# Optimization experiments

Measured on AMD Instinct MI355X. Metric: run time of the kernel, lower is better.

## Reference

```python
import jax, jax.numpy as jnp
from jax import lax
import numpy as np

B, DIM, H, W = 8, 192, 128, 128
HEADS = 4


def setup_inputs() -> dict:
    key = jax.random.key(0)
    k1, k2, k3, k4 = jax.random.split(key, 4)
    x = jax.random.normal(k1, (B, DIM, H, W), dtype=jnp.float32)
    w_qkv = jax.random.normal(k2, (2 * DIM, DIM), dtype=jnp.float32) * 0.05
    w_dw = jax.random.normal(k3, (2 * DIM, 1, 3, 3), dtype=jnp.float32) * 0.1
    w_proj = jax.random.normal(k4, (DIM, DIM), dtype=jnp.float32) * 0.05
    temperature = jnp.ones((HEADS, 1, 1), dtype=jnp.float32)
    return {"x": x, "w_qkv": w_qkv, "w_dw": w_dw, "w_proj": w_proj, "temperature": temperature}


def reference(x, w_qkv, w_dw, w_proj, temperature):
    b, c, h, w = x.shape
    heads = temperature.shape[0]
    head_c = c // heads
    # 1x1 conv: dim -> 2*dim
    qkv = jnp.einsum('oc,bchw->bohw', w_qkv, x)
    # 3x3 depthwise conv over 2*dim channels
    qkv = lax.conv_general_dilated(
        qkv, w_dw, window_strides=(1, 1), padding='SAME',
        feature_group_count=2 * c,
        dimension_numbers=('NCHW', 'OIHW', 'NCHW'))
    q, v = jnp.split(qkv, 2, axis=1)
    # [b, heads, head_c, h*w]
    q = q.reshape(b, heads, head_c, h * w)
    v = v.reshape(b, heads, head_c, h * w)
    # L2-normalize q over spatial dim; k = q
    q = q / jnp.linalg.norm(q, axis=-1, keepdims=True)
    # channel-wise attention: [b, heads, head_c, head_c]
    attn = jnp.einsum('bhcn,bhdn->bhcd', q, q) * temperature[None]
    attn = jax.nn.softmax(attn, axis=-1)
    out = jnp.einsum('bhcd,bhdn->bhcn', attn, v)
    out = out.reshape(b, c, h, w)
    # 1x1 projection
    return jnp.einsum('oc,bchw->bohw', w_proj, out)
```

## Files before the change

kernel.cpp:

```cpp
#include <hip/hip_runtime.h>

#define BB 8
#define CC 192
#define C2 384
#define HH 128
#define WW 128
#define NN 16384
#define NHEADS 4
#define HC 48
#define LTK 196
#define LTK2 98

typedef float f32x4 __attribute__((ext_vector_type(4)));
typedef float f32x16 __attribute__((ext_vector_type(16)));
typedef short s16x4 __attribute__((ext_vector_type(4)));
typedef short s16x8 __attribute__((ext_vector_type(8)));
typedef unsigned short u16;
typedef u16 u16x4 __attribute__((ext_vector_type(4)));
typedef u16 u16x8 __attribute__((ext_vector_type(8)));
typedef unsigned int u32;

__device__ __forceinline__ float bfu2f(u32 u16v) {
  return __uint_as_float(u16v << 16);
}
__device__ __forceinline__ u16 f2bfu(float f) {
  u32 u = __float_as_uint(f);
  return (u16)((u + 0x7fffu + ((u >> 16) & 1u)) >> 16);
}
__device__ __forceinline__ s16x8 ldpair(const u16* p) {
  s16x4 lo = *reinterpret_cast<const s16x4*>(p);
  s16x4 hi = *reinterpret_cast<const s16x4*>(p + 16);
  return __builtin_shufflevector(lo, hi, 0, 1, 2, 3, 4, 5, 6, 7);
}
__device__ __forceinline__ s16x8 ldb64pair(const u32* p) {
  s16x4 lo = *reinterpret_cast<const s16x4*>(p);
  s16x4 hi = *reinterpret_cast<const s16x4*>(p + 2);
  return __builtin_shufflevector(lo, hi, 0, 1, 2, 3, 4, 5, 6, 7);
}

__global__ __launch_bounds__(256) void k0_wcvt(const float* __restrict__ w,
                                               u16* __restrict__ wbf) {
  const int i = (blockIdx.x * 256 + threadIdx.x) * 4;
  f32x4 v = *reinterpret_cast<const f32x4*>(&w[i]);
  u16x4 o;
  o[0] = f2bfu(v[0]); o[1] = f2bfu(v[1]); o[2] = f2bfu(v[2]); o[3] = f2bfu(v[3]);
  *reinterpret_cast<u16x4*>(&wbf[i]) = o;
}

__global__ __launch_bounds__(512, 4) void k1_qkv(
    const float* __restrict__ x, const u16* __restrict__ wbf,
    u16* __restrict__ qkv) {
  const int bx = blockIdx.x;
  const int n0 = (((bx & 7) << 4) + (bx >> 3)) << 7;
  const int b  = blockIdx.y;
  __shared__ u16 Xs[128 * LTK];
  u32* Xsw = reinterpret_cast<u32*>(Xs);
  const int t = threadIdx.x, lane = t & 63;
  const int wid = t >> 6, wo = wid >> 1, wn = wid & 1;
  const int l31 = lane & 31, g2 = lane >> 5;

  {
    const int nq = t & 31, cr = t >> 5;
    const int kpb = cr >> 1;
    const int jh = cr & 1;
    const int prA = 2 * nq + jh;
    const int prB = 64 + 2 * nq + jh;
    const float* xb = x + (size_t)b * CC * NN + n0 + 4 * nq;
    #pragma unroll 6
    for (int i = 0; i < 12; ++i) {
      f32x4 v = *reinterpret_cast<const f32x4*>(xb + (size_t)(cr + 16 * i) * NN);
      u32 A  = (u32)f2bfu(v[0]) | ((u32)f2bfu(v[1]) << 16);
      u32 Bp = (u32)f2bfu(v[2]) | ((u32)f2bfu(v[3]) << 16);
      u32 oA = __shfl_xor(A, 32);
      u32 oB = __shfl_xor(Bp, 32);
      u32 va, vb;
      if (jh) {
        va = (oB & 0xffffu) | (Bp << 16);
        vb = (oB >> 16) | (Bp & 0xffff0000u);
      } else {
        va = (A & 0xffffu) | (oA << 16);
        vb = (A >> 16) | (oA & 0xffff0000u);
      }
      const int col = kpb + 8 * i;
      Xsw[prA * LTK2 + col] = va;
      Xsw[prB * LTK2 + col] = vb;
    }
  }
  __syncthreads();

  const int nb2 = wn * 32;
  const u32* browE = &Xsw[(nb2 + l31) * LTK2 + 4 * g2];
  const u32* browO = &Xsw[(64 + nb2 + l31) * LTK2 + 4 * g2];

  for (int ot = 0; ot < 3; ++ot) {
    const int o0 = ot * 128;
    const u16* wr = wbf + (size_t)(o0 + wo * 32 + l31) * CC + 8 * g2;

    s16x8 afA[6], afB[6];
    #pragma unroll
    for (int s = 0; s < 6; ++s) {
      afA[s] = *reinterpret_cast<const s16x8*>(wr + s * 32);
      afB[s] = *reinterpret_cast<const s16x8*>(wr + s * 32 + 16);
    }

    f32x16 accE, accO;
    #pragma unroll
    for (int e = 0; e < 16; ++e) { accE[e] = 0.f; accO[e] = 0.f; }

    #pragma unroll
    for (int s = 0; s < 6; ++s) {
      s16x8 bfE0 = ldb64pair(browE + 16 * s);
      s16x8 bfE1 = ldb64pair(browE + 16 * s + 8);
      s16x8 bfO0 = ldb64pair(browO + 16 * s);
      s16x8 bfO1 = ldb64pair(browO + 16 * s + 8);
      accE = __builtin_amdgcn_mfma_f32_32x32x16_bf16(afA[s], bfE0, accE, 0, 0, 0);
      accO = __builtin_amdgcn_mfma_f32_32x32x16_bf16(afA[s], bfO0, accO, 0, 0, 0);
      accE = __builtin_amdgcn_mfma_f32_32x32x16_bf16(afB[s], bfE1, accE, 0, 0, 0);
      accO = __builtin_amdgcn_mfma_f32_32x32x16_bf16(afB[s], bfO1, accO, 0, 0, 0);
    }
    #pragma unroll
    for (int r = 0; r < 16; ++r) {
      const int row = (r & 3) + 8 * (r >> 2) + 4 * g2;
      const u32 pk = (u32)f2bfu(accE[r]) | ((u32)f2bfu(accO[r]) << 16);
      *reinterpret_cast<u32*>(
          &qkv[((size_t)b * C2 + o0 + wo * 32 + row) * NN + n0 + wn * 64 + 2 * l31]) = pk;
    }
  }
}

__global__ __launch_bounds__(256) void k2_dw(
    const u16* __restrict__ qkv, const float* __restrict__ wdw,
    u16* __restrict__ out) {
  const int gid = blockIdx.x;
  const int rb = gid & 7;
  const int plane = gid >> 3;
  const int ch = plane % C2;
  const int t = threadIdx.x;
  const int row = rb * 16 + (t >> 4);
  const int x0 = (t & 15) * 8;
  const u16* p = qkv + (size_t)plane * NN;
  const float* wv = wdw + ch * 9;
  float o[8];
  #pragma unroll
  for (int j = 0; j < 8; ++j) o[j] = 0.f;
  #pragma unroll
  for (int dy = 0; dy < 3; ++dy) {
    const int yy = row + dy - 1;
    if ((unsigned)yy < (unsigned)HH) {
      const u16* rp = p + yy * WW;
      u16x8 m = *reinterpret_cast<const u16x8*>(&rp[x0]);
      float px[10];
      px[0] = (x0 > 0) ? bfu2f(rp[x0 - 1]) : 0.f;
      px[9] = (x0 < 120) ? bfu2f(rp[x0 + 8]) : 0.f;
      #pragma unroll
      for (int j = 0; j < 8; ++j) px[j + 1] = bfu2f(m[j]);
      const float w0 = wv[dy * 3 + 0], w1 = wv[dy * 3 + 1], w2 = wv[dy * 3 + 2];
      #pragma unroll
      for (int j = 0; j < 8; ++j)
        o[j] += w0 * px[j] + w1 * px[j + 1] + w2 * px[j + 2];
    }
  }
  u16x8 ov;
  #pragma unroll
  for (int j = 0; j < 8; ++j) ov[j] = f2bfu(o[j]);
  *reinterpret_cast<u16x8*>(&out[(size_t)plane * NN + row * WW + x0]) = ov;
}

__global__ __launch_bounds__(256) void k3_gram(
    const u16* __restrict__ qkvd, float* __restrict__ gpart) {
  const int bh = blockIdx.x, b = bh >> 2, h = bh & 3;
  const int chunk = blockIdx.y;
  const int t = threadIdx.x, lane = t & 63, wv = t >> 6;
  const int l15 = lane & 15, g = lane >> 4;
  __shared__ float red[4][2304];
  const u16* qb = qkvd + ((size_t)b * C2 + h * HC) * NN;

  f32x4 acc[3][3];
  #pragma unroll
  for (int i = 0; i < 3; ++i)
    #pragma unroll
    for (int j = 0; j < 3; ++j)
      #pragma unroll
      for (int e = 0; e < 4; ++e) acc[i][j][e] = 0.f;

  const int nbase = chunk * 1024 + wv * 256;
  #pragma unroll 2
  for (int st = 0; st < 8; ++st) {
    const int n = nbase + st * 32;
    s16x8 cf[3];
    #pragma unroll
    for (int i = 0; i < 3; ++i)
      cf[i] = ldpair(qb + (size_t)(i * 16 + l15) * NN + n + 4 * g);
    #pragma unroll
    for (int i = 0; i < 3; ++i)
      #pragma unroll
      for (int j = 0; j < 3; ++j)
        acc[i][j] = __builtin_amdgcn_mfma_f32_16x16x32_bf16(cf[i], cf[j], acc[i][j], 0, 0, 0);
  }
  #pragma unroll
  for (int i = 0; i < 3; ++i)
    #pragma unroll
    for (int j = 0; j < 3; ++j)
      #pragma unroll
      for (int r = 0; r < 4; ++r)
        red[wv][(i * 16 + 4 * g + r) * 48 + j * 16 + l15] = acc[i][j][r];
  __syncthreads();
  float* gp = gpart + ((size_t)bh * 16 + chunk) * 2304;
  for (int idx = t; idx < 2304; idx += 256)
    gp[idx] = red[0][idx] + red[1][idx] + red[2][idx] + red[3][idx];
}

__global__ __launch_bounds__(256) void k4_soft(
    const float* __restrict__ gpart, const float* __restrict__ temp,
    float* __restrict__ attn) {
  const int bh = blockIdx.x;
  const int h = bh & 3;
  const int t = threadIdx.x;
  __shared__ float G[2304];
  __shared__ float rn[48];
  for (int idx = t; idx < 2304; idx += 256) {
    float s = 0.f;
    #pragma unroll
    for (int c = 0; c < 16; ++c) s += gpart[((size_t)bh * 16 + c) * 2304 + idx];
    G[idx] = s;
  }
  __syncthreads();
  if (t < 48) rn[t] = rsqrtf(G[t * 48 + t]);
  __syncthreads();
  if (t < 48) {
    const float tm = temp[h];
    float v[48];
    float mx = -1e30f;
    #pragma unroll
    for (int j = 0; j < 48; ++j) {
      v[j] = G[t * 48 + j] * rn[t] * rn[j] * tm;
      mx = fmaxf(mx, v[j]);
    }
    float s = 0.f;
    #pragma unroll
    for (int j = 0; j < 48; ++j) { v[j] = expf(v[j] - mx); s += v[j]; }
    const float inv = 1.f / s;
    #pragma unroll
    for (int j = 0; j < 48; ++j)
      attn[(size_t)bh * 2304 + t * 48 + j] = v[j] * inv;
  }
}

__global__ __launch_bounds__(192) void k5_M(
    const float* __restrict__ wproj, const float* __restrict__ attn,
    u16* __restrict__ Mbf) {
  const int o = blockIdx.x;
  const int b = blockIdx.y;
  const int d = threadIdx.x;
  const int h = d / HC, dl = d % HC;
  const float* wrow = wproj + o * CC + h * HC;
  const float* at = attn + ((size_t)(b * NHEADS + h)) * 2304;
  float s = 0.f;
  #pragma unroll
  for (int c = 0; c < HC; ++c) s = fmaf(wrow[c], at[c * HC + dl], s);
  Mbf[((size_t)b * CC + o) * CC + d] = f2bfu(s);
}

__global__ __launch_bounds__(256, 4) void k6_out(
    const u16* __restrict__ Mbf, const u16* __restrict__ qkvd,
    float* __restrict__ out) {
  const int bx = blockIdx.x;
  const int n0 = (((bx & 7) << 4) + (bx >> 3)) << 7;
  const int b  = blockIdx.y;
  __shared__ u16 Vs[128 * LTK];
  u32* Vsw = reinterpret_cast<u32*>(Vs);
  const int t = threadIdx.x, lane = t & 63;
  const int wid = t >> 6, wo = wid >> 1, wn = wid & 1;
  const int l31 = lane & 31, g2 = lane >> 5;

  {
    const int nq = t & 31, cr = t >> 5;
    const int kpb = cr >> 1;
    const int jh = cr & 1;
    const int prA = 2 * nq + jh;
    const int prB = 64 + 2 * nq + jh;
    const u16* vbp = qkvd + ((size_t)b * C2 + CC) * NN + n0 + 4 * nq;
    #pragma unroll 6
    for (int i = 0; i < 24; ++i) {
      u16x4 m = *reinterpret_cast<const u16x4*>(vbp + (size_t)(cr + 8 * i) * NN);
      u32 A  = (u32)m[0] | ((u32)m[1] << 16);
      u32 Bp = (u32)m[2] | ((u32)m[3] << 16);
      u32 oA = __shfl_xor(A, 32);
      u32 oB = __shfl_xor(Bp, 32);
      u32 va, vb;
      if (jh) {
        va = (oB & 0xffffu) | (Bp << 16);
        vb = (oB >> 16) | (Bp & 0xffff0000u);
      } else {
        va = (A & 0xffffu) | (oA << 16);
        vb = (A >> 16) | (oA & 0xffff0000u);
      }
      const int col = kpb + 4 * i;
      Vsw[prA * LTK2 + col] = va;
      Vsw[prB * LTK2 + col] = vb;
    }
  }
  __syncthreads();

  const int nb2 = wn * 32;
  const u32* browE = &Vsw[(nb2 + l31) * LTK2 + 4 * g2];
  const u32* browO = &Vsw[(64 + nb2 + l31) * LTK2 + 4 * g2];
  const u16* Ab = Mbf + (size_t)b * CC * CC;

  for (int ot = 0; ot < 3; ++ot) {
    const int o0 = ot * 64;
    const u16* ar = Ab + (size_t)(o0 + wo * 32 + l31) * CC + 8 * g2;

    s16x8 afA[6], afB[6];
    #pragma unroll
    for (int s = 0; s < 6; ++s) {
      afA[s] = *reinterpret_cast<const s16x8*>(ar + s * 32);
      afB[s] = *reinterpret_cast<const s16x8*>(ar + s * 32 + 16);
    }

    f32x16 accE, accO;
    #pragma unroll
    for (int e = 0; e < 16; ++e) { accE[e] = 0.f; accO[e] = 0.f; }

    #pragma unroll
    for (int s = 0; s < 6; ++s) {
      s16x8 bfE0 = ldb64pair(browE + 16 * s);
      s16x8 bfE1 = ldb64pair(browE + 16 * s + 8);
      s16x8 bfO0 = ldb64pair(browO + 16 * s);
      s16x8 bfO1 = ldb64pair(browO + 16 * s + 8);
      accE = __builtin_amdgcn_mfma_f32_32x32x16_bf16(afA[s], bfE0, accE, 0, 0, 0);
      accO = __builtin_amdgcn_mfma_f32_32x32x16_bf16(afA[s], bfO0, accO, 0, 0, 0);
      accE = __builtin_amdgcn_mfma_f32_32x32x16_bf16(afB[s], bfE1, accE, 0, 0, 0);
      accO = __builtin_amdgcn_mfma_f32_32x32x16_bf16(afB[s], bfO1, accO, 0, 0, 0);
    }
    #pragma unroll
    for (int r = 0; r < 16; ++r) {
      const int row = (r & 3) + 8 * (r >> 2) + 4 * g2;
      float2 st;
      st.x = accE[r];
      st.y = accO[r];
      *reinterpret_cast<float2*>(
          &out[((size_t)b * CC + o0 + wo * 32 + row) * NN + n0 + wn * 64 + 2 * l31]) = st;
    }
  }
}

extern "C" void kernel_launch(void* const* d_in, const int* in_sizes, int n_in,
                              void* d_out, int out_size, void* d_ws, size_t ws_size,
                              hipStream_t stream) {
  const float* x      = (const float*)d_in[0];
  const float* w_qkv  = (const float*)d_in[1];
  const float* w_dw   = (const float*)d_in[2];
  const float* w_proj = (const float*)d_in[3];
  const float* temp   = (const float*)d_in[4];
  float* out = (float*)d_out;

  const size_t OFF_QKV   = 0;
  const size_t OFF_QKVD  = 100663296ULL;
  const size_t OFF_GPART = 201326592ULL;
  const size_t OFF_ATTN  = 206045184ULL;
  const size_t OFF_M     = 206340096ULL;
  const size_t OFF_WBF   = 206929920ULL;
  const size_t NEEDED    = 207077376ULL;
  if (ws_size < NEEDED) return;

  char* ws = (char*)d_ws;
  u16* qkv   = (u16*)(ws + OFF_QKV);
  u16* qkvd  = (u16*)(ws + OFF_QKVD);
  float* gpart = (float*)(ws + OFF_GPART);
  float* attn  = (float*)(ws + OFF_ATTN);
  u16* Mbf   = (u16*)(ws + OFF_M);
  u16* wbf   = (u16*)(ws + OFF_WBF);

  k0_wcvt<<<dim3(72), 256, 0, stream>>>(w_qkv, wbf);
  k1_qkv <<<dim3(128, 8), 512, 0, stream>>>(x, wbf, qkv);
  k2_dw  <<<dim3(BB * C2 * 8), 256, 0, stream>>>(qkv, w_dw, qkvd);
  k3_gram<<<dim3(BB * NHEADS, 16), 256, 0, stream>>>(qkvd, gpart);
  k4_soft<<<dim3(BB * NHEADS), 256, 0, stream>>>(gpart, temp, attn);
  k5_M   <<<dim3(CC, BB), 192, 0, stream>>>(w_proj, attn, Mbf);
  k6_out <<<dim3(128, 8), 256, 0, stream>>>(Mbf, qkvd, out);
}
```

Before: 214.8 us.

## Double k1 spatial tile to 256 columns with 1024-thread blocks and simpler staging

The QKV 1x1-conv kernel now processes 256 spatial positions per block with 16 waves instead of 128 positions with 8 waves, halving the grid. This spreads each weight-fragment load over twice as many columns. The X staging loop is rewritten to load two channel rows per thread and pack channel pairs directly, which removes the cross-lane shuffles. In exchange, LDS use per block doubles to about 100KB, which limits occupancy to one block per CU, and the grid of 512 blocks may fill the GPU less evenly.

```diff
diff --git a/kernel.cpp b/kernel.cpp
--- a/kernel.cpp
+++ b/kernel.cpp
@@ -47,50 +47,41 @@
   *reinterpret_cast<u16x4*>(&wbf[i]) = o;
 }
 
-__global__ __launch_bounds__(512, 4) void k1_qkv(
+__global__ __launch_bounds__(1024, 4) void k1_qkv(
     const float* __restrict__ x, const u16* __restrict__ wbf,
     u16* __restrict__ qkv) {
   const int bx = blockIdx.x;
-  const int n0 = (((bx & 7) << 4) + (bx >> 3)) << 7;
+  const int n0 = (((bx & 7) << 3) + (bx >> 3)) << 8;
   const int b  = blockIdx.y;
-  __shared__ u16 Xs[128 * LTK];
+  __shared__ u16 Xs[256 * LTK];
   u32* Xsw = reinterpret_cast<u32*>(Xs);
   const int t = threadIdx.x, lane = t & 63;
-  const int wid = t >> 6, wo = wid >> 1, wn = wid & 1;
+  const int wid = t >> 6, wo = wid >> 2, wn = wid & 3;
   const int l31 = lane & 31, g2 = lane >> 5;
 
   {
-    const int nq = t & 31, cr = t >> 5;
-    const int kpb = cr >> 1;
-    const int jh = cr & 1;
-    const int prA = 2 * nq + jh;
-    const int prB = 64 + 2 * nq + jh;
-    const float* xb = x + (size_t)b * CC * NN + n0 + 4 * nq;
-    #pragma unroll 6
-    for (int i = 0; i < 12; ++i) {
-      f32x4 v = *reinterpret_cast<const f32x4*>(xb + (size_t)(cr + 16 * i) * NN);
-      u32 A  = (u32)f2bfu(v[0]) | ((u32)f2bfu(v[1]) << 16);
-      u32 Bp = (u32)f2bfu(v[2]) | ((u32)f2bfu(v[3]) << 16);
-      u32 oA = __shfl_xor(A, 32);
-      u32 oB = __shfl_xor(Bp, 32);
-      u32 va, vb;
-      if (jh) {
-        va = (oB & 0xffffu) | (Bp << 16);
-        vb = (oB >> 16) | (Bp & 0xffff0000u);
-      } else {
-        va = (A & 0xffffu) | (oA << 16);
-        vb = (A >> 16) | (oA & 0xffff0000u);
-      }
-      const int col = kpb + 8 * i;
-      Xsw[prA * LTK2 + col] = va;
-      Xsw[prB * LTK2 + col] = vb;
-    }
-  }
-  __syncthreads();
-
-  const int nb2 = wn * 32;
-  const u32* browE = &Xsw[(nb2 + l31) * LTK2 + 4 * g2];
-  const u32* browO = &Xsw[(64 + nb2 + l31) * LTK2 + 4 * g2];
+    const int q = t & 63;
+    const int pb = t >> 6;
+    const float* xb = x + (size_t)b * CC * NN + n0 + 4 * q;
+    #pragma unroll
+    for (int i = 0; i < 6; ++i) {
+      const int p = pb + 16 * i;
+      f32x4 r0 = *reinterpret_cast<const f32x4*>(xb + (size_t)(2 * p) * NN);
+      f32x4 r1 = *reinterpret_cast<const f32x4*>(xb + (size_t)(2 * p + 1) * NN);
+      u32 w0 = (u32)f2bfu(r0[0]) | ((u32)f2bfu(r1[0]) << 16);
+      u32 w1 = (u32)f2bfu(r0[1]) | ((u32)f2bfu(r1[1]) << 16);
+      u32 w2 = (u32)f2bfu(r0[2]) | ((u32)f2bfu(r1[2]) << 16);
+      u32 w3 = (u32)f2bfu(r0[3]) | ((u32)f2bfu(r1[3]) << 16);
+      Xsw[(2 * q) * LTK2 + p]       = w0;
+      Xsw[(2 * q + 128) * LTK2 + p] = w1;
+      Xsw[(2 * q + 1) * LTK2 + p]   = w2;
+      Xsw[(2 * q + 129) * LTK2 + p] = w3;
+    }
+  }
+  __syncthreads();
+
+  const u32* browE = &Xsw[(wn * 32 + l31) * LTK2 + 4 * g2];
+  const u32* browO = &Xsw[(128 + wn * 32 + l31) * LTK2 + 4 * g2];
 
   for (int ot = 0; ot < 3; ++ot) {
     const int o0 = ot * 128;
@@ -373,7 +364,7 @@
   u16* wbf   = (u16*)(ws + OFF_WBF);
 
   k0_wcvt<<<dim3(72), 256, 0, stream>>>(w_qkv, wbf);
-  k1_qkv <<<dim3(128, 8), 512, 0, stream>>>(x, wbf, qkv);
+  k1_qkv <<<dim3(64, 8), 1024, 0, stream>>>(x, wbf, qkv);
   k2_dw  <<<dim3(BB * C2 * 8), 256, 0, stream>>>(qkv, w_dw, qkvd);
   k3_gram<<<dim3(BB * NHEADS, 16), 256, 0, stream>>>(qkvd, gpart);
   k4_soft<<<dim3(BB * NHEADS), 256, 0, stream>>>(gpart, temp, attn);
```

Measured after the change: 213.8 us. Within noise of the previous version (-0.5%).

## Fuse q-half depthwise conv into Gram kernel via LDS tiles

Applied to the files above, without the earlier changes.

Adds a kernel that loads a row-band halo of the q channels into shared memory, applies the 3x3 depthwise conv there, and feeds the result straight into the bf16 MFMA Gram accumulation. This removes the global write and re-read of the convolved q tensor. The old depthwise kernel now handles only the v channels. Gram partials are stored per 2-row band (64 per head) in the unused q region of the workspace. The softmax kernel therefore reduces more partials, and each input row is read twice because of the halo. The final output stores also switch to nontemporal stores.

```diff
diff --git a/kernel.cpp b/kernel.cpp
--- a/kernel.cpp
+++ b/kernel.cpp
@@ -11,6 +11,7 @@
 #define LTK 196
 #define LTK2 98
 
+typedef float f32x2 __attribute__((ext_vector_type(2)));
 typedef float f32x4 __attribute__((ext_vector_type(4)));
 typedef float f32x16 __attribute__((ext_vector_type(16)));
 typedef short s16x4 __attribute__((ext_vector_type(4)));
@@ -133,12 +134,14 @@
     u16* __restrict__ out) {
   const int gid = blockIdx.x;
   const int rb = gid & 7;
-  const int plane = gid >> 3;
-  const int ch = plane % C2;
+  const int p = gid >> 3;
+  const int b = p / 192, cv = p % 192;
+  const int ch = CC + cv;
+  const int plane = b * C2 + ch;
   const int t = threadIdx.x;
   const int row = rb * 16 + (t >> 4);
   const int x0 = (t & 15) * 8;
-  const u16* p = qkv + (size_t)plane * NN;
+  const u16* pp = qkv + (size_t)plane * NN;
   const float* wv = wdw + ch * 9;
   float o[8];
   #pragma unroll
@@ -147,7 +150,7 @@
   for (int dy = 0; dy < 3; ++dy) {
     const int yy = row + dy - 1;
     if ((unsigned)yy < (unsigned)HH) {
-      const u16* rp = p + yy * WW;
+      const u16* rp = pp + yy * WW;
       u16x8 m = *reinterpret_cast<const u16x8*>(&rp[x0]);
       float px[10];
       px[0] = (x0 > 0) ? bfu2f(rp[x0 - 1]) : 0.f;
@@ -166,14 +169,66 @@
   *reinterpret_cast<u16x8*>(&out[(size_t)plane * NN + row * WW + x0]) = ov;
 }
 
-__global__ __launch_bounds__(256) void k3_gram(
-    const u16* __restrict__ qkvd, float* __restrict__ gpart) {
-  const int bh = blockIdx.x, b = bh >> 2, h = bh & 3;
-  const int chunk = blockIdx.y;
+__global__ __launch_bounds__(256, 2) void k23_convgram(
+    const u16* __restrict__ qkv, const float* __restrict__ wdw,
+    float* __restrict__ gpart) {
+  const int raw = blockIdx.x;
+  const int rp = ((raw & 7) << 3) + (raw >> 3);
+  const int h = blockIdx.y, b = blockIdx.z;
+  __shared__ u16 inq[48 * 520];
+  __shared__ float wsm[432];
+  __shared__ u16 qd[48 * 264];
   const int t = threadIdx.x, lane = t & 63, wv = t >> 6;
   const int l15 = lane & 15, g = lane >> 4;
-  __shared__ float red[4][2304];
-  const u16* qb = qkvd + ((size_t)b * C2 + h * HC) * NN;
+  const u16* qb = qkv + ((size_t)b * C2 + h * HC) * NN;
+
+  for (int idx = t; idx < 432; idx += 256) wsm[idx] = wdw[h * 432 + idx];
+  #pragma unroll
+  for (int it = 0; it < 12; ++it) {
+    const int idx = t + 256 * it;
+    const int ch = idx >> 6, rem = idx & 63;
+    const int iy = rem >> 4, grp = rem & 15;
+    const int gy = 2 * rp - 1 + iy;
+    u16x8 v;
+    #pragma unroll
+    for (int e = 0; e < 8; ++e) v[e] = 0;
+    if ((unsigned)gy < (unsigned)HH)
+      v = *reinterpret_cast<const u16x8*>(qb + (size_t)ch * NN + gy * WW + grp * 8);
+    *reinterpret_cast<u16x8*>(&inq[ch * 520 + iy * 128 + grp * 8]) = v;
+  }
+  __syncthreads();
+
+  #pragma unroll
+  for (int it = 0; it < 6; ++it) {
+    const int idx = t + 256 * it;
+    const int ch = idx >> 5, grp = idx & 31;
+    const int p0 = grp * 8;
+    const int orow = p0 >> 7, x0 = p0 & 127;
+    float o[8];
+    #pragma unroll
+    for (int j = 0; j < 8; ++j) o[j] = 0.f;
+    #pragma unroll
+    for (int dy = 0; dy < 3; ++dy) {
+      const u16* rp_ = &inq[ch * 520 + (orow + dy) * 128];
+      u16x8 m = *reinterpret_cast<const u16x8*>(&rp_[x0]);
+      float px[10];
+      px[0] = (x0 > 0) ? bfu2f(rp_[x0 - 1]) : 0.f;
+      px[9] = (x0 < 120) ? bfu2f(rp_[x0 + 8]) : 0.f;
+      #pragma unroll
+      for (int j = 0; j < 8; ++j) px[j + 1] = bfu2f(m[j]);
+      const float w0 = wsm[ch * 9 + dy * 3 + 0];
+      const float w1 = wsm[ch * 9 + dy * 3 + 1];
+      const float w2 = wsm[ch * 9 + dy * 3 + 2];
+      #pragma unroll
+      for (int j = 0; j < 8; ++j)
+        o[j] += w0 * px[j] + w1 * px[j + 1] + w2 * px[j + 2];
+    }
+    u16x8 ov;
+    #pragma unroll
+    for (int j = 0; j < 8; ++j) ov[j] = f2bfu(o[j]);
+    *reinterpret_cast<u16x8*>(&qd[ch * 264 + p0]) = ov;
+  }
+  __syncthreads();
 
   f32x4 acc[3][3];
   #pragma unroll
@@ -183,45 +238,47 @@
       #pragma unroll
       for (int e = 0; e < 4; ++e) acc[i][j][e] = 0.f;
 
-  const int nbase = chunk * 1024 + wv * 256;
-  #pragma unroll 2
-  for (int st = 0; st < 8; ++st) {
-    const int n = nbase + st * 32;
+  #pragma unroll
+  for (int s = 0; s < 2; ++s) {
+    const int n = wv * 64 + s * 32;
     s16x8 cf[3];
     #pragma unroll
     for (int i = 0; i < 3; ++i)
-      cf[i] = ldpair(qb + (size_t)(i * 16 + l15) * NN + n + 4 * g);
+      cf[i] = ldpair(&qd[(i * 16 + l15) * 264 + n + 4 * g]);
     #pragma unroll
     for (int i = 0; i < 3; ++i)
       #pragma unroll
       for (int j = 0; j < 3; ++j)
         acc[i][j] = __builtin_amdgcn_mfma_f32_16x16x32_bf16(cf[i], cf[j], acc[i][j], 0, 0, 0);
   }
+
+  float* red = reinterpret_cast<float*>(inq);
   #pragma unroll
   for (int i = 0; i < 3; ++i)
     #pragma unroll
     for (int j = 0; j < 3; ++j)
       #pragma unroll
       for (int r = 0; r < 4; ++r)
-        red[wv][(i * 16 + 4 * g + r) * 48 + j * 16 + l15] = acc[i][j][r];
-  __syncthreads();
-  float* gp = gpart + ((size_t)bh * 16 + chunk) * 2304;
+        red[wv * 2304 + (i * 16 + 4 * g + r) * 48 + j * 16 + l15] = acc[i][j][r];
+  __syncthreads();
+  float* gp = gpart + (size_t)b * 3145728 + h * 147456 + rp * 2304;
   for (int idx = t; idx < 2304; idx += 256)
-    gp[idx] = red[0][idx] + red[1][idx] + red[2][idx] + red[3][idx];
+    gp[idx] = red[idx] + red[2304 + idx] + red[4608 + idx] + red[6912 + idx];
 }
 
 __global__ __launch_bounds__(256) void k4_soft(
     const float* __restrict__ gpart, const float* __restrict__ temp,
     float* __restrict__ attn) {
   const int bh = blockIdx.x;
-  const int h = bh & 3;
+  const int b = bh >> 2, h = bh & 3;
   const int t = threadIdx.x;
   __shared__ float G[2304];
   __shared__ float rn[48];
+  const float* gp = gpart + (size_t)b * 3145728 + h * 147456;
   for (int idx = t; idx < 2304; idx += 256) {
     float s = 0.f;
-    #pragma unroll
-    for (int c = 0; c < 16; ++c) s += gpart[((size_t)bh * 16 + c) * 2304 + idx];
+    #pragma unroll 8
+    for (int c = 0; c < 64; ++c) s += gp[c * 2304 + idx];
     G[idx] = s;
   }
   __syncthreads();
@@ -336,11 +393,12 @@
     #pragma unroll
     for (int r = 0; r < 16; ++r) {
       const int row = (r & 3) + 8 * (r >> 2) + 4 * g2;
-      float2 st;
-      st.x = accE[r];
-      st.y = accO[r];
-      *reinterpret_cast<float2*>(
-          &out[((size_t)b * CC + o0 + wo * 32 + row) * NN + n0 + wn * 64 + 2 * l31]) = st;
+      f32x2 st;
+      st[0] = accE[r];
+      st[1] = accO[r];
+      f32x2* op = reinterpret_cast<f32x2*>(
+          &out[((size_t)b * CC + o0 + wo * 32 + row) * NN + n0 + wn * 64 + 2 * l31]);
+      __builtin_nontemporal_store(st, op);
     }
   }
 }
@@ -357,7 +415,6 @@
 
   const size_t OFF_QKV   = 0;
   const size_t OFF_QKVD  = 100663296ULL;
-  const size_t OFF_GPART = 201326592ULL;
   const size_t OFF_ATTN  = 206045184ULL;
   const size_t OFF_M     = 206340096ULL;
   const size_t OFF_WBF   = 206929920ULL;
@@ -367,15 +424,15 @@
   char* ws = (char*)d_ws;
   u16* qkv   = (u16*)(ws + OFF_QKV);
   u16* qkvd  = (u16*)(ws + OFF_QKVD);
-  float* gpart = (float*)(ws + OFF_GPART);
+  float* gpart = (float*)(ws + OFF_QKVD);
   float* attn  = (float*)(ws + OFF_ATTN);
   u16* Mbf   = (u16*)(ws + OFF_M);
   u16* wbf   = (u16*)(ws + OFF_WBF);
 
   k0_wcvt<<<dim3(72), 256, 0, stream>>>(w_qkv, wbf);
   k1_qkv <<<dim3(128, 8), 512, 0, stream>>>(x, wbf, qkv);
-  k2_dw  <<<dim3(BB * C2 * 8), 256, 0, stream>>>(qkv, w_dw, qkvd);
-  k3_gram<<<dim3(BB * NHEADS, 16), 256, 0, stream>>>(qkvd, gpart);
+  k2_dw  <<<dim3(BB * 192 * 8), 256, 0, stream>>>(qkv, w_dw, qkvd);
+  k23_convgram<<<dim3(64, NHEADS, BB), 256, 0, stream>>>(qkv, w_dw, gpart);
   k4_soft<<<dim3(BB * NHEADS), 256, 0, stream>>>(gpart, temp, attn);
   k5_M   <<<dim3(CC, BB), 192, 0, stream>>>(w_proj, attn, Mbf);
   k6_out <<<dim3(128, 8), 256, 0, stream>>>(Mbf, qkvd, out);
```

New measurement: 223.6 us. +4.1%, slower.

## Make k1 and k6 persistent with double-buffered LDS prefetch across four tiles

Applied to the files above, without the earlier changes.

k1_qkv and k6_out now launch 256 blocks that each process four consecutive 128-pixel tiles. The next tile's global loads are issued into registers before the current tile's MFMA work, then written to a second LDS buffer. This overlaps global load latency with compute. k6 moves to 512 threads covering the 192 outputs in two passes (one partially idle) and uses nontemporal stores for the fp32 output. The costs are more registers and LDS, lower occupancy, and fewer blocks per GPU.

```diff
diff --git a/kernel.cpp b/kernel.cpp
--- a/kernel.cpp
+++ b/kernel.cpp
@@ -11,6 +11,7 @@
 #define LTK 196
 #define LTK2 98
 
+typedef float f32x2 __attribute__((ext_vector_type(2)));
 typedef float f32x4 __attribute__((ext_vector_type(4)));
 typedef float f32x16 __attribute__((ext_vector_type(16)));
 typedef short s16x4 __attribute__((ext_vector_type(4)));
@@ -47,28 +48,30 @@
   *reinterpret_cast<u16x4*>(&wbf[i]) = o;
 }
 
-__global__ __launch_bounds__(512, 4) void k1_qkv(
+__global__ __launch_bounds__(512, 1) void k1_qkv(
     const float* __restrict__ x, const u16* __restrict__ wbf,
     u16* __restrict__ qkv) {
-  const int bx = blockIdx.x;
-  const int n0 = (((bx & 7) << 4) + (bx >> 3)) << 7;
-  const int b  = blockIdx.y;
-  __shared__ u16 Xs[128 * LTK];
-  u32* Xsw = reinterpret_cast<u32*>(Xs);
+  const int bid = blockIdx.x;
+  const int base = (((bid & 7) << 5) + (bid >> 3)) << 2;
+  __shared__ u16 Xs[2][128 * LTK];
   const int t = threadIdx.x, lane = t & 63;
   const int wid = t >> 6, wo = wid >> 1, wn = wid & 1;
   const int l31 = lane & 31, g2 = lane >> 5;
-
+  const int nq = t & 31, cr = t >> 5;
+  const int kpb = cr >> 1, jh = cr & 1;
+  const int prA = 2 * nq + jh, prB = 64 + 2 * nq + jh;
+
+  f32x4 ld[12];
   {
-    const int nq = t & 31, cr = t >> 5;
-    const int kpb = cr >> 1;
-    const int jh = cr & 1;
-    const int prA = 2 * nq + jh;
-    const int prB = 64 + 2 * nq + jh;
-    const float* xb = x + (size_t)b * CC * NN + n0 + 4 * nq;
-    #pragma unroll 6
+    const int b = base >> 7, p0 = base & 127;
+    const float* xb = x + (size_t)b * CC * NN + (p0 << 7) + 4 * nq;
+    #pragma unroll
+    for (int i = 0; i < 12; ++i)
+      ld[i] = *reinterpret_cast<const f32x4*>(xb + (size_t)(cr + 16 * i) * NN);
+    u32* Xw = reinterpret_cast<u32*>(&Xs[0][0]);
+    #pragma unroll
     for (int i = 0; i < 12; ++i) {
-      f32x4 v = *reinterpret_cast<const f32x4*>(xb + (size_t)(cr + 16 * i) * NN);
+      f32x4 v = ld[i];
       u32 A  = (u32)f2bfu(v[0]) | ((u32)f2bfu(v[1]) << 16);
       u32 Bp = (u32)f2bfu(v[2]) | ((u32)f2bfu(v[3]) << 16);
       u32 oA = __shfl_xor(A, 32);
@@ -81,49 +84,81 @@
         va = (A & 0xffffu) | (oA << 16);
         vb = (A >> 16) | (oA & 0xffff0000u);
       }
-      const int col = kpb + 8 * i;
-      Xsw[prA * LTK2 + col] = va;
-      Xsw[prB * LTK2 + col] = vb;
+      Xw[prA * LTK2 + kpb + 8 * i] = va;
+      Xw[prB * LTK2 + kpb + 8 * i] = vb;
     }
   }
   __syncthreads();
 
-  const int nb2 = wn * 32;
-  const u32* browE = &Xsw[(nb2 + l31) * LTK2 + 4 * g2];
-  const u32* browO = &Xsw[(64 + nb2 + l31) * LTK2 + 4 * g2];
-
-  for (int ot = 0; ot < 3; ++ot) {
-    const int o0 = ot * 128;
-    const u16* wr = wbf + (size_t)(o0 + wo * 32 + l31) * CC + 8 * g2;
-
-    s16x8 afA[6], afB[6];
-    #pragma unroll
-    for (int s = 0; s < 6; ++s) {
-      afA[s] = *reinterpret_cast<const s16x8*>(wr + s * 32);
-      afB[s] = *reinterpret_cast<const s16x8*>(wr + s * 32 + 16);
-    }
-
-    f32x16 accE, accO;
-    #pragma unroll
-    for (int e = 0; e < 16; ++e) { accE[e] = 0.f; accO[e] = 0.f; }
-
-    #pragma unroll
-    for (int s = 0; s < 6; ++s) {
-      s16x8 bfE0 = ldb64pair(browE + 16 * s);
-      s16x8 bfE1 = ldb64pair(browE + 16 * s + 8);
-      s16x8 bfO0 = ldb64pair(browO + 16 * s);
-      s16x8 bfO1 = ldb64pair(browO + 16 * s + 8);
-      accE = __builtin_amdgcn_mfma_f32_32x32x16_bf16(afA[s], bfE0, accE, 0, 0, 0);
-      accO = __builtin_amdgcn_mfma_f32_32x32x16_bf16(afA[s], bfO0, accO, 0, 0, 0);
-      accE = __builtin_amdgcn_mfma_f32_32x32x16_bf16(afB[s], bfE1, accE, 0, 0, 0);
-      accO = __builtin_amdgcn_mfma_f32_32x32x16_bf16(afB[s], bfO1, accO, 0, 0, 0);
-    }
-    #pragma unroll
-    for (int r = 0; r < 16; ++r) {
-      const int row = (r & 3) + 8 * (r >> 2) + 4 * g2;
-      const u32 pk = (u32)f2bfu(accE[r]) | ((u32)f2bfu(accO[r]) << 16);
-      *reinterpret_cast<u32*>(
-          &qkv[((size_t)b * C2 + o0 + wo * 32 + row) * NN + n0 + wn * 64 + 2 * l31]) = pk;
+  for (int j = 0; j < 4; ++j) {
+    const int lin = base + j;
+    const int b = lin >> 7, p0 = lin & 127;
+    if (j < 3) {
+      const int lin2 = lin + 1;
+      const int b2 = lin2 >> 7, p2 = lin2 & 127;
+      const float* xb = x + (size_t)b2 * CC * NN + (p2 << 7) + 4 * nq;
+      #pragma unroll
+      for (int i = 0; i < 12; ++i)
+        ld[i] = *reinterpret_cast<const f32x4*>(xb + (size_t)(cr + 16 * i) * NN);
+    }
+    const u32* Xsw = reinterpret_cast<const u32*>(&Xs[j & 1][0]);
+    const u32* browE = &Xsw[(wn * 32 + l31) * LTK2 + 4 * g2];
+    const u32* browO = &Xsw[(64 + wn * 32 + l31) * LTK2 + 4 * g2];
+    u16* qbase = qkv + (size_t)b * C2 * NN + (p0 << 7);
+
+    for (int ot = 0; ot < 3; ++ot) {
+      const int o0 = ot * 128;
+      const u16* wr = wbf + (size_t)(o0 + wo * 32 + l31) * CC + 8 * g2;
+      s16x8 afA[6], afB[6];
+      #pragma unroll
+      for (int s = 0; s < 6; ++s) {
+        afA[s] = *reinterpret_cast<const s16x8*>(wr + s * 32);
+        afB[s] = *reinterpret_cast<const s16x8*>(wr + s * 32 + 16);
+      }
+      f32x16 accE, accO;
+      #pragma unroll
+      for (int e = 0; e < 16; ++e) { accE[e] = 0.f; accO[e] = 0.f; }
+      #pragma unroll
+      for (int s = 0; s < 6; ++s) {
+        s16x8 bfE0 = ldb64pair(browE + 16 * s);
+        s16x8 bfE1 = ldb64pair(browE + 16 * s + 8);
+        s16x8 bfO0 = ldb64pair(browO + 16 * s);
+        s16x8 bfO1 = ldb64pair(browO + 16 * s + 8);
+        accE = __builtin_amdgcn_mfma_f32_32x32x16_bf16(afA[s], bfE0, accE, 0, 0, 0);
+        accO = __builtin_amdgcn_mfma_f32_32x32x16_bf16(afA[s], bfO0, accO, 0, 0, 0);
+        accE = __builtin_amdgcn_mfma_f32_32x32x16_bf16(afB[s], bfE1, accE, 0, 0, 0);
+        accO = __builtin_amdgcn_mfma_f32_32x32x16_bf16(afB[s], bfO1, accO, 0, 0, 0);
+      }
+      #pragma unroll
+      for (int r = 0; r < 16; ++r) {
+        const int row = (r & 3) + 8 * (r >> 2) + 4 * g2;
+        const u32 pk = (u32)f2bfu(accE[r]) | ((u32)f2bfu(accO[r]) << 16);
+        *reinterpret_cast<u32*>(
+            &qbase[(size_t)(o0 + wo * 32 + row) * NN + wn * 64 + 2 * l31]) = pk;
+      }
+    }
+    if (j < 3) {
+      __syncthreads();
+      u32* Xw = reinterpret_cast<u32*>(&Xs[(j + 1) & 1][0]);
+      #pragma unroll
+      for (int i = 0; i < 12; ++i) {
+        f32x4 v = ld[i];
+        u32 A  = (u32)f2bfu(v[0]) | ((u32)f2bfu(v[1]) << 16);
+        u32 Bp = (u32)f2bfu(v[2]) | ((u32)f2bfu(v[3]) << 16);
+        u32 oA = __shfl_xor(A, 32);
+        u32 oB = __shfl_xor(Bp, 32);
+        u32 va, vb;
+        if (jh) {
+          va = (oB & 0xffffu) | (Bp << 16);
+          vb = (oB >> 16) | (Bp & 0xffff0000u);
+        } else {
+          va = (A & 0xffffu) | (oA << 16);
+          vb = (A >> 16) | (oA & 0xffff0000u);
+        }
+        Xw[prA * LTK2 + kpb + 8 * i] = va;
+        Xw[prB * LTK2 + kpb + 8 * i] = vb;
+      }
+      __syncthreads();
     }
   }
 }
@@ -261,28 +296,30 @@
   Mbf[((size_t)b * CC + o) * CC + d] = f2bfu(s);
 }
 
-__global__ __launch_bounds__(256, 4) void k6_out(
+__global__ __launch_bounds__(512, 1) void k6_out(
     const u16* __restrict__ Mbf, const u16* __restrict__ qkvd,
     float* __restrict__ out) {
-  const int bx = blockIdx.x;
-  const int n0 = (((bx & 7) << 4) + (bx >> 3)) << 7;
-  const int b  = blockIdx.y;
-  __shared__ u16 Vs[128 * LTK];
-  u32* Vsw = reinterpret_cast<u32*>(Vs);
+  const int bid = blockIdx.x;
+  const int base = (((bid & 7) << 5) + (bid >> 3)) << 2;
+  __shared__ u16 Vs[2][128 * LTK];
   const int t = threadIdx.x, lane = t & 63;
   const int wid = t >> 6, wo = wid >> 1, wn = wid & 1;
   const int l31 = lane & 31, g2 = lane >> 5;
-
+  const int nq = t & 31, cr = t >> 5;
+  const int kpb = cr >> 1, jh = cr & 1;
+  const int prA = 2 * nq + jh, prB = 64 + 2 * nq + jh;
+
+  u16x4 ld[12];
   {
-    const int nq = t & 31, cr = t >> 5;
-    const int kpb = cr >> 1;
-    const int jh = cr & 1;
-    const int prA = 2 * nq + jh;
-    const int prB = 64 + 2 * nq + jh;
-    const u16* vbp = qkvd + ((size_t)b * C2 + CC) * NN + n0 + 4 * nq;
-    #pragma unroll 6
-    for (int i = 0; i < 24; ++i) {
-      u16x4 m = *reinterpret_cast<const u16x4*>(vbp + (size_t)(cr + 8 * i) * NN);
+    const int b = base >> 7, p0 = base & 127;
+    const u16* vbp = qkvd + ((size_t)b * C2 + CC) * NN + (p0 << 7) + 4 * nq;
+    #pragma unroll
+    for (int i = 0; i < 12; ++i)
+      ld[i] = *reinterpret_cast<const u16x4*>(vbp + (size_t)(cr + 16 * i) * NN);
+    u32* Vw = reinterpret_cast<u32*>(&Vs[0][0]);
+    #pragma unroll
+    for (int i = 0; i < 12; ++i) {
+      u16x4 m = ld[i];
       u32 A  = (u32)m[0] | ((u32)m[1] << 16);
       u32 Bp = (u32)m[2] | ((u32)m[3] << 16);
       u32 oA = __shfl_xor(A, 32);
@@ -295,52 +332,89 @@
         va = (A & 0xffffu) | (oA << 16);
         vb = (A >> 16) | (oA & 0xffff0000u);
       }
-      const int col = kpb + 4 * i;
-      Vsw[prA * LTK2 + col] = va;
-      Vsw[prB * LTK2 + col] = vb;
+      Vw[prA * LTK2 + kpb + 8 * i] = va;
+      Vw[prB * LTK2 + kpb + 8 * i] = vb;
     }
   }
   __syncthreads();
 
-  const int nb2 = wn * 32;
-  const u32* browE = &Vsw[(nb2 + l31) * LTK2 + 4 * g2];
-  const u32* browO = &Vsw[(64 + nb2 + l31) * LTK2 + 4 * g2];
-  const u16* Ab = Mbf + (size_t)b * CC * CC;
-
-  for (int ot = 0; ot < 3; ++ot) {
-    const int o0 = ot * 64;
-    const u16* ar = Ab + (size_t)(o0 + wo * 32 + l31) * CC + 8 * g2;
-
-    s16x8 afA[6], afB[6];
-    #pragma unroll
-    for (int s = 0; s < 6; ++s) {
-      afA[s] = *reinterpret_cast<const s16x8*>(ar + s * 32);
-      afB[s] = *reinterpret_cast<const s16x8*>(ar + s * 32 + 16);
-    }
-
-    f32x16 accE, accO;
-    #pragma unroll
-    for (int e = 0; e < 16; ++e) { accE[e] = 0.f; accO[e] = 0.f; }
-
-    #pragma unroll
-    for (int s = 0; s < 6; ++s) {
-      s16x8 bfE0 = ldb64pair(browE + 16 * s);
-      s16x8 bfE1 = ldb64pair(browE + 16 * s + 8);
-      s16x8 bfO0 = ldb64pair(browO + 16 * s);
-      s16x8 bfO1 = ldb64pair(browO + 16 * s + 8);
-      accE = __builtin_amdgcn_mfma_f32_32x32x16_bf16(afA[s], bfE0, accE, 0, 0, 0);
-      accO = __builtin_amdgcn_mfma_f32_32x32x16_bf16(afA[s], bfO0, accO, 0, 0, 0);
-      accE = __builtin_amdgcn_mfma_f32_32x32x16_bf16(afB[s], bfE1, accE, 0, 0, 0);
-      accO = __builtin_amdgcn_mfma_f32_32x32x16_bf16(afB[s], bfO1, accO, 0, 0, 0);
-    }
-    #pragma unroll
-    for (int r = 0; r < 16; ++r) {
-      const int row = (r & 3) + 8 * (r >> 2) + 4 * g2;
-      float2 st;
-      st.x = accE[r];
-      st.y = accO[r];
-      *reinterpret_cast<float2*>(
-          &out[((size_t)b * CC + o0 + wo * 32 + row) * NN + n0 + wn * 64 + 2 * l31]) = st;
+  for (int j = 0; j < 4; ++j) {
+    const int lin = base + j;
+    const int b = lin >> 7, p0 = lin & 127;
+    if (j < 3) {
+      const int lin2 = lin + 1;
+      const int b2 = lin2 >> 7, p2 = lin2 & 127;
+      const u16* vbp = qkvd + ((size_t)b2 * C2 + CC) * NN + (p2 << 7) + 4 * nq;
+      #pragma unroll
+      for (int i = 0; i < 12; ++i)
+        ld[i] = *reinterpret_cast<const u16x4*>(vbp + (size_t)(cr + 16 * i) * NN);
+    }
+    const u32* Vsw = reinterpret_cast<const u32*>(&Vs[j & 1][0]);
+    const u32* browE = &Vsw[(wn * 32 + l31) * LTK2 + 4 * g2];
+    const u32* browO = &Vsw[(64 + wn * 32 + l31) * LTK2 + 4 * g2];
+    const u16* Ab = Mbf + (size_t)b * CC * CC;
+    float* obase = out + (size_t)b * CC * NN + (p0 << 7);
+
+    #pragma unroll
+    for (int ot = 0; ot < 2; ++ot) {
+      const int o0 = ot * 128;
+      const bool active = (ot == 0) || (wo < 2);
+      if (active) {
+        const u16* ar = Ab + (size_t)(o0 + wo * 32 + l31) * CC + 8 * g2;
+        s16x8 afA[6], afB[6];
+        #pragma unroll
+        for (int s = 0; s < 6; ++s) {
+          afA[s] = *reinterpret_cast<const s16x8*>(ar + s * 32);
+          afB[s] = *reinterpret_cast<const s16x8*>(ar + s * 32 + 16);
+        }
+        f32x16 accE, accO;
+        #pragma unroll
+        for (int e = 0; e < 16; ++e) { accE[e] = 0.f; accO[e] = 0.f; }
+        #pragma unroll
+        for (int s = 0; s < 6; ++s) {
+          s16x8 bfE0 = ldb64pair(browE + 16 * s);
+          s16x8 bfE1 = ldb64pair(browE + 16 * s + 8);
+          s16x8 bfO0 = ldb64pair(browO + 16 * s);
+          s16x8 bfO1 = ldb64pair(browO + 16 * s + 8);
+          accE = __builtin_amdgcn_mfma_f32_32x32x16_bf16(afA[s], bfE0, accE, 0, 0, 0);
+          accO = __builtin_amdgcn_mfma_f32_32x32x16_bf16(afA[s], bfO0, accO, 0, 0, 0);
+          accE = __builtin_amdgcn_mfma_f32_32x32x16_bf16(afB[s], bfE1, accE, 0, 0, 0);
+          accO = __builtin_amdgcn_mfma_f32_32x32x16_bf16(afB[s], bfO1, accO, 0, 0, 0);
+        }
+        #pragma unroll
+        for (int r = 0; r < 16; ++r) {
+          const int row = (r & 3) + 8 * (r >> 2) + 4 * g2;
+          f32x2 st;
+          st[0] = accE[r];
+          st[1] = accO[r];
+          f32x2* op = reinterpret_cast<f32x2*>(
+              &obase[(size_t)(o0 + wo * 32 + row) * NN + wn * 64 + 2 * l31]);
+          __builtin_nontemporal_store(st, op);
+        }
+      }
+    }
+    if (j < 3) {
+      __syncthreads();
+      u32* Vw = reinterpret_cast<u32*>(&Vs[(j + 1) & 1][0]);
+      #pragma unroll
+      for (int i = 0; i < 12; ++i) {
+        u16x4 m = ld[i];
+        u32 A  = (u32)m[0] | ((u32)m[1] << 16);
+        u32 Bp = (u32)m[2] | ((u32)m[3] << 16);
+        u32 oA = __shfl_xor(A, 32);
+        u32 oB = __shfl_xor(Bp, 32);
+        u32 va, vb;
+        if (jh) {
+          va = (oB & 0xffffu) | (Bp << 16);
+          vb = (oB >> 16) | (Bp & 0xffff0000u);
+        } else {
+          va = (A & 0xffffu) | (oA << 16);
+          vb = (A >> 16) | (oA & 0xffff0000u);
+        }
+        Vw[prA * LTK2 + kpb + 8 * i] = va;
+        Vw[prB * LTK2 + kpb + 8 * i] = vb;
+      }
+      __syncthreads();
     }
   }
 }
@@ -373,10 +447,10 @@
   u16* wbf   = (u16*)(ws + OFF_WBF);
 
   k0_wcvt<<<dim3(72), 256, 0, stream>>>(w_qkv, wbf);
-  k1_qkv <<<dim3(128, 8), 512, 0, stream>>>(x, wbf, qkv);
+  k1_qkv <<<dim3(256), 512, 0, stream>>>(x, wbf, qkv);
   k2_dw  <<<dim3(BB * C2 * 8), 256, 0, stream>>>(qkv, w_dw, qkvd);
   k3_gram<<<dim3(BB * NHEADS, 16), 256, 0, stream>>>(qkvd, gpart);
   k4_soft<<<dim3(BB * NHEADS), 256, 0, stream>>>(gpart, temp, attn);
   k5_M   <<<dim3(CC, BB), 192, 0, stream>>>(w_proj, attn, Mbf);
-  k6_out <<<dim3(128, 8), 256, 0, stream>>>(Mbf, qkvd, out);
-}
+  k6_out <<<dim3(256), 512, 0, stream>>>(Mbf, qkvd, out);
+}
```

Measured after the change: 226.4 us. 1.05x slower.
